# Kernel tuning notes

Hardware: AMD Instinct MI355X
Metric: run time of the kernel (lower is better)

Reference implementation:

```python
import jax, jax.numpy as jnp
import numpy as np

DIM = 4096
BATCH = 8192
LAYERS = int(np.log2(DIM))  # 12


def _butterfly_indices(dim):
    lefts, rights = [], []
    for l in range(int(np.log2(dim))):
        stride = 1 << l
        starts = np.arange(0, dim, 2 * stride)[:, None]
        offs = np.arange(stride)[None, :]
        left = (starts + offs).reshape(-1)
        lefts.append(left)
        rights.append(left + stride)
    return np.stack(lefts), np.stack(rights)  # (layers, dim//2)


def setup_inputs() -> dict:
    key = jax.random.key(0)
    kx, ka = jax.random.split(key)
    x = jax.random.normal(kx, (BATCH, DIM), dtype=jnp.float32)
    # angles ~ Uniform(-0.05, 0.05), one per pair per layer
    angles = jax.random.uniform(ka, (LAYERS, DIM // 2), dtype=jnp.float32,
                                minval=-0.05, maxval=0.05)
    li, ri = _butterfly_indices(DIM)
    left_idx = jnp.asarray(li, dtype=jnp.int64) if jax.config.jax_enable_x64 else jnp.asarray(li, dtype=jnp.int32)
    right_idx = jnp.asarray(ri, dtype=left_idx.dtype)
    return {"x": x, "angles": angles, "left_idx": left_idx, "right_idx": right_idx}


def reference(x, angles, left_idx, right_idx):
    # x: (B, D); angles/left_idx/right_idx: (layers, D//2)
    y = x
    for l in range(angles.shape[0]):  # fixed small loop over log2(D) layers
        c = jnp.cos(angles[l])  # (D//2,)
        s = jnp.sin(angles[l])
        xl = jnp.take(y, left_idx[l], axis=1)   # (B, D//2)
        xr = jnpp_take(y, right_idx[l]) if False else jnp.take(y, right_idx[l], axis=1)
        new_left = xl * c + xr * s
        new_right = -xl * s + xr * c
        # left/right indices partition [0, D), so the scatter fully overwrites y
        y = jnp.zeros_like(y).at[:, left_idx[l]].set(new_left).at[:, right_idx[l]].set(new_right)
    return y
```

## Files before the change

kernel.cpp:

```cpp
#include <hip/hip_runtime.h>
#include <hip/hip_fp16.h>
#include <cmath>


namespace {
constexpr int kDim = 4096;
constexpr int kBatch = 8192;
constexpr int kLayers = 12;
constexpr int kPairs = kDim / 2;
constexpr int kThreads = 256;
constexpr int kLdsWords = kDim + 4 * (kDim / 64);
}

__device__ __forceinline__ int lds_pad(int i) { return i + ((i >> 6) << 2); }

__device__ __forceinline__ int slot_to_pair(int l, int t, int q) {
    const int m = l & 3;
    const int phase = l >> 2;
    const int j = ((q >> m) << (m + 1)) | (q & ((1 << m) - 1));
    int i;
    if (phase == 0)      i = 16 * t + j;
    else if (phase == 1) i = (t & 15) + 16 * j + 256 * (t >> 4);
    else                 i = t + 256 * j;
    const int s = 1 << l;
    return ((i >> (l + 1)) << l) | (i & (s - 1));
}

__global__ void bf_precompute(const float* __restrict__ angles,
                              __half2* __restrict__ tab) {
    const int k = blockIdx.x * blockDim.x + threadIdx.x;
    if (k >= kLayers * kPairs) return;
    const int l = k >> 11;
    const int slot = k & 2047;
    const int t = slot >> 3;
    const int q = slot & 7;
    const int p = slot_to_pair(l, t, q);
    const float a = angles[l * kPairs + p];
    tab[k] = __floats2half2_rn(sinf(a), cosf(a) - 1.0f);
}

__device__ __forceinline__ void apply_phase(float (&v)[16], const uint4 (&tb)[8]) {
#pragma unroll
    for (int m = 0; m < 4; ++m) {
        const __half2* h = reinterpret_cast<const __half2*>(&tb[2 * m]);
#pragma unroll
        for (int q = 0; q < 8; ++q) {
            const int j = ((q >> m) << (m + 1)) | (q & ((1 << m) - 1));
            const int jp = j + (1 << m);
            const float2 sc = __half22float2(h[q]);
            const float s = sc.x, cm1 = sc.y;
            const float xl = v[j], xr = v[jp];
            v[j]  = fmaf(xl, cm1, fmaf(xr,  s, xl));
            v[jp] = fmaf(xr, cm1, fmaf(-xl, s, xr));
        }
    }
}

__global__ __launch_bounds__(kThreads, 8)
void bf_butterfly(const float* __restrict__ x,
                  const __half2* __restrict__ tab,
                  float* __restrict__ out) {
    __shared__ float lds[kLdsWords];
    const int t = threadIdx.x;
    const int low = t & 15, high = t >> 4;
    const int baseA = 16 * t + 4 * (t >> 2);
    const int base1 = low + 272 * high;
    const int base2 = t + 4 * (t >> 6);
    const int row = blockIdx.x;

    const uint4* ap = reinterpret_cast<const uint4*>(tab);

    uint4 tb[8];
#pragma unroll
    for (int m = 0; m < 4; ++m) {
        tb[2 * m]     = ap[m * 512 + 2 * t];
        tb[2 * m + 1] = ap[m * 512 + 2 * t + 1];
    }

    float v[16];
    {
        const float4* src = reinterpret_cast<const float4*>(x + (size_t)row * kDim + 16 * t);
#pragma unroll
        for (int k = 0; k < 4; ++k) {
            const float4 f = src[k];
            v[4 * k + 0] = f.x; v[4 * k + 1] = f.y;
            v[4 * k + 2] = f.z; v[4 * k + 3] = f.w;
        }
    }

    apply_phase(v, tb);

#pragma unroll
    for (int k = 0; k < 4; ++k) {
        *reinterpret_cast<float4*>(&lds[baseA + 4 * k]) =
            make_float4(v[4 * k], v[4 * k + 1], v[4 * k + 2], v[4 * k + 3]);
    }

#pragma unroll
    for (int m = 0; m < 4; ++m) {
        tb[2 * m]     = ap[(4 + m) * 512 + 2 * t];
        tb[2 * m + 1] = ap[(4 + m) * 512 + 2 * t + 1];
    }

    __syncthreads();
#pragma unroll
    for (int j = 0; j < 16; ++j) {
        v[j] = lds[base1 + 16 * j + 4 * (j >> 2)];
    }

    apply_phase(v, tb);

#pragma unroll
    for (int j = 0; j < 16; ++j) {
        lds[base1 + 16 * j + 4 * (j >> 2)] = v[j];
    }

#pragma unroll
    for (int m = 0; m < 4; ++m) {
        tb[2 * m]     = ap[(8 + m) * 512 + 2 * t];
        tb[2 * m + 1] = ap[(8 + m) * 512 + 2 * t + 1];
    }

    __syncthreads();
#pragma unroll
    for (int j = 0; j < 16; ++j) {
        v[j] = lds[base2 + 272 * j];
    }

    apply_phase(v, tb);

    float* dst = out + (size_t)row * kDim;
#pragma unroll
    for (int j = 0; j < 16; ++j) {
        __builtin_nontemporal_store(v[j], dst + t + 256 * j);
    }
}

extern "C" void kernel_launch(void* const* d_in, const int* in_sizes, int n_in,
                              void* d_out, int out_size, void* d_ws, size_t ws_size,
                              hipStream_t stream) {
    (void)in_sizes; (void)n_in; (void)out_size; (void)ws_size;
    const float* x = (const float*)d_in[0];
    const float* angles = (const float*)d_in[1];
    __half2* tab = (__half2*)d_ws;
    float* out = (float*)d_out;

    bf_precompute<<<(kLayers * kPairs + kThreads - 1) / kThreads, kThreads, 0, stream>>>(
        angles, tab);
    bf_butterfly<<<kBatch, kThreads, 0, stream>>>(x, tab, out);
}
```

Baseline: 257.3 us.

## Use wavefront shuffles for middle butterfly layers and reduce LDS exchanges

Layers 4-9 are now done with cross-lane xor shuffles within each 64-lane wavefront instead of LDS transposes, leaving a single LDS exchange before the last two layers. The twiddle table is re-laid out so each stage reads it in the order threads need. Output stores become vectorized float4 nontemporal stores. This cuts barriers and LDS traffic, but adds many shuffle instructions and more per-thread table loads.

```diff
diff --git a/kernel.cpp b/kernel.cpp
--- a/kernel.cpp
+++ b/kernel.cpp
@@ -6,80 +6,66 @@
 namespace {
 constexpr int kDim = 4096;
 constexpr int kBatch = 8192;
-constexpr int kLayers = 12;
 constexpr int kPairs = kDim / 2;
 constexpr int kThreads = 256;
-constexpr int kLdsWords = kDim + 4 * (kDim / 64);
+constexpr int kTabB = 2048;
+constexpr int kTabC = 5120;
+constexpr int kTabTotal = 6144;
 }
 
-__device__ __forceinline__ int lds_pad(int i) { return i + ((i >> 6) << 2); }
-
-__device__ __forceinline__ int slot_to_pair(int l, int t, int q) {
-    const int m = l & 3;
-    const int phase = l >> 2;
-    const int j = ((q >> m) << (m + 1)) | (q & ((1 << m) - 1));
-    int i;
-    if (phase == 0)      i = 16 * t + j;
-    else if (phase == 1) i = (t & 15) + 16 * j + 256 * (t >> 4);
-    else                 i = t + 256 * j;
-    const int s = 1 << l;
-    return ((i >> (l + 1)) << l) | (i & (s - 1));
-}
+typedef float float4v __attribute__((ext_vector_type(4)));
 
 __global__ void bf_precompute(const float* __restrict__ angles,
                               __half2* __restrict__ tab) {
-    const int k = blockIdx.x * blockDim.x + threadIdx.x;
-    if (k >= kLayers * kPairs) return;
-    const int l = k >> 11;
-    const int slot = k & 2047;
-    const int t = slot >> 3;
-    const int q = slot & 7;
-    const int p = slot_to_pair(l, t, q);
+    const int h = blockIdx.x * blockDim.x + threadIdx.x;
+    if (h >= kTabTotal * 4) return;
+    const int idx = h >> 2;
+    const int pos = h & 3;
+    int l, i;
+    if (idx < kTabB) {
+        l = idx >> 9;
+        const int r = idx & 511;
+        const int u = r >> 8, t = r & 255;
+        const int q = u * 4 + pos;
+        const int j = ((q >> l) << (l + 1)) | (q & ((1 << l) - 1));
+        i = 16 * t + j;
+    } else if (idx < kTabC) {
+        const int e = idx - kTabB;
+        const int b = e >> 9;
+        l = 4 + b;
+        const int r = e & 511;
+        const int u = r >> 7, row = r & 127;
+        const int k = u * 4 + pos;
+        const int t0 = ((row >> b) << (b + 1)) | (row & ((1 << b) - 1));
+        i = 16 * t0 + k;
+    } else {
+        const int e = idx - kTabC;
+        l = 10 + (e >> 9);
+        const int r = e & 511;
+        const int u = r >> 8, t = r & 255;
+        const int q = u * 4 + pos;
+        const int j = (l == 10) ? (((q >> 2) << 3) | (q & 3)) : q;
+        i = 4 * t + (j & 3) + 1024 * (j >> 2);
+    }
+    const int s = 1 << l;
+    const int p = ((i >> (l + 1)) << l) | (i & (s - 1));
     const float a = angles[l * kPairs + p];
-    tab[k] = __floats2half2_rn(sinf(a), cosf(a) - 1.0f);
-}
-
-__device__ __forceinline__ void apply_phase(float (&v)[16], const uint4 (&tb)[8]) {
-#pragma unroll
-    for (int m = 0; m < 4; ++m) {
-        const __half2* h = reinterpret_cast<const __half2*>(&tb[2 * m]);
-#pragma unroll
-        for (int q = 0; q < 8; ++q) {
-            const int j = ((q >> m) << (m + 1)) | (q & ((1 << m) - 1));
-            const int jp = j + (1 << m);
-            const float2 sc = __half22float2(h[q]);
-            const float s = sc.x, cm1 = sc.y;
-            const float xl = v[j], xr = v[jp];
-            v[j]  = fmaf(xl, cm1, fmaf(xr,  s, xl));
-            v[jp] = fmaf(xr, cm1, fmaf(-xl, s, xr));
-        }
-    }
+    tab[h] = __floats2half2_rn(sinf(a), cosf(a) - 1.0f);
 }
 
 __global__ __launch_bounds__(kThreads, 8)
 void bf_butterfly(const float* __restrict__ x,
                   const __half2* __restrict__ tab,
                   float* __restrict__ out) {
-    __shared__ float lds[kLdsWords];
+    __shared__ float lds[kDim];
     const int t = threadIdx.x;
-    const int low = t & 15, high = t >> 4;
-    const int baseA = 16 * t + 4 * (t >> 2);
-    const int base1 = low + 272 * high;
-    const int base2 = t + 4 * (t >> 6);
     const int row = blockIdx.x;
-
     const uint4* ap = reinterpret_cast<const uint4*>(tab);
-
-    uint4 tb[8];
-#pragma unroll
-    for (int m = 0; m < 4; ++m) {
-        tb[2 * m]     = ap[m * 512 + 2 * t];
-        tb[2 * m + 1] = ap[m * 512 + 2 * t + 1];
-    }
 
     float v[16];
     {
-        const float4* src = reinterpret_cast<const float4*>(x + (size_t)row * kDim + 16 * t);
+        const float4* src =
+            reinterpret_cast<const float4*>(x + (size_t)row * kDim + 16 * t);
 #pragma unroll
         for (int k = 0; k < 4; ++k) {
             const float4 f = src[k];
@@ -88,51 +74,79 @@
         }
     }
 
-    apply_phase(v, tb);
+#pragma unroll
+    for (int l = 0; l < 4; ++l) {
+        uint4 ta[2];
+        ta[0] = ap[l * 512 + t];
+        ta[1] = ap[l * 512 + 256 + t];
+        const __half2* hh = reinterpret_cast<const __half2*>(ta);
+#pragma unroll
+        for (int q = 0; q < 8; ++q) {
+            const int j  = ((q >> l) << (l + 1)) | (q & ((1 << l) - 1));
+            const int jp = j + (1 << l);
+            const float2 sc = __half22float2(hh[q]);
+            const float s = sc.x, cm1 = sc.y;
+            const float xl = v[j], xr = v[jp];
+            v[j]  = fmaf(xl, cm1, fmaf(xr,  s, xl));
+            v[jp] = fmaf(xr, cm1, fmaf(-xl, s, xr));
+        }
+    }
+
+#pragma unroll
+    for (int b = 0; b < 6; ++b) {
+        const int m = 1 << b;
+        const int rw = ((t >> (b + 1)) << b) | (t & (m - 1));
+        uint4 tb[4];
+#pragma unroll
+        for (int u = 0; u < 4; ++u) tb[u] = ap[kTabB + b * 512 + u * 128 + rw];
+        const __half2* hh = reinterpret_cast<const __half2*>(tb);
+        const unsigned sgn = (((unsigned)t >> b) & 1u) << 31;
+#pragma unroll
+        for (int k = 0; k < 16; ++k) {
+            const float2 sc = __half22float2(hh[k]);
+            const float se = __uint_as_float(__float_as_uint(sc.x) ^ sgn);
+            const float rv = __shfl_xor(v[k], m, 64);
+            v[k] = fmaf(rv, se, fmaf(v[k], sc.y, v[k]));
+        }
+    }
 
 #pragma unroll
     for (int k = 0; k < 4; ++k) {
-        *reinterpret_cast<float4*>(&lds[baseA + 4 * k]) =
+        *reinterpret_cast<float4*>(&lds[16 * t + 4 * k]) =
             make_float4(v[4 * k], v[4 * k + 1], v[4 * k + 2], v[4 * k + 3]);
+    }
+    __syncthreads();
+#pragma unroll
+    for (int g = 0; g < 4; ++g) {
+        const float4 f = *reinterpret_cast<const float4*>(&lds[4 * t + 1024 * g]);
+        v[4 * g + 0] = f.x; v[4 * g + 1] = f.y;
+        v[4 * g + 2] = f.z; v[4 * g + 3] = f.w;
     }
 
 #pragma unroll
-    for (int m = 0; m < 4; ++m) {
-        tb[2 * m]     = ap[(4 + m) * 512 + 2 * t];
-        tb[2 * m + 1] = ap[(4 + m) * 512 + 2 * t + 1];
+    for (int lc = 0; lc < 2; ++lc) {
+        uint4 tc[2];
+        tc[0] = ap[kTabC + lc * 512 + t];
+        tc[1] = ap[kTabC + lc * 512 + 256 + t];
+        const __half2* hh = reinterpret_cast<const __half2*>(tc);
+#pragma unroll
+        for (int q = 0; q < 8; ++q) {
+            const int j  = (lc == 0) ? (((q >> 2) << 3) | (q & 3)) : q;
+            const int jp = j + ((lc == 0) ? 4 : 8);
+            const float2 sc = __half22float2(hh[q]);
+            const float s = sc.x, cm1 = sc.y;
+            const float xl = v[j], xr = v[jp];
+            v[j]  = fmaf(xl, cm1, fmaf(xr,  s, xl));
+            v[jp] = fmaf(xr, cm1, fmaf(-xl, s, xr));
+        }
     }
 
-    __syncthreads();
+    float* dst = out + (size_t)row * kDim + 4 * t;
 #pragma unroll
-    for (int j = 0; j < 16; ++j) {
-        v[j] = lds[base1 + 16 * j + 4 * (j >> 2)];
-    }
-
-    apply_phase(v, tb);
-
-#pragma unroll
-    for (int j = 0; j < 16; ++j) {
-        lds[base1 + 16 * j + 4 * (j >> 2)] = v[j];
-    }
-
-#pragma unroll
-    for (int m = 0; m < 4; ++m) {
-        tb[2 * m]     = ap[(8 + m) * 512 + 2 * t];
-        tb[2 * m + 1] = ap[(8 + m) * 512 + 2 * t + 1];
-    }
-
-    __syncthreads();
-#pragma unroll
-    for (int j = 0; j < 16; ++j) {
-        v[j] = lds[base2 + 272 * j];
-    }
-
-    apply_phase(v, tb);
-
-    float* dst = out + (size_t)row * kDim;
-#pragma unroll
-    for (int j = 0; j < 16; ++j) {
-        __builtin_nontemporal_store(v[j], dst + t + 256 * j);
+    for (int g = 0; g < 4; ++g) {
+        float4v f;
+        f.x = v[4 * g]; f.y = v[4 * g + 1]; f.z = v[4 * g + 2]; f.w = v[4 * g + 3];
+        __builtin_nontemporal_store(f, reinterpret_cast<float4v*>(dst + 1024 * g));
     }
 }
 
@@ -145,7 +159,8 @@
     __half2* tab = (__half2*)d_ws;
     float* out = (float*)d_out;
 
-    bf_precompute<<<(kLayers * kPairs + kThreads - 1) / kThreads, kThreads, 0, stream>>>(
+    const int nHalf2 = kTabTotal * 4;
+    bf_precompute<<<(nHalf2 + kThreads - 1) / kThreads, kThreads, 0, stream>>>(
         angles, tab);
     bf_butterfly<<<kBatch, kThreads, 0, stream>>>(x, tab, out);
 }
```

Result: slower. 465.6 us (+80.9%).
